# Kernel tuning notes

Hardware: AMD Instinct MI355X
Metric: run time of the kernel (lower is better)

## Reference

```python
import jax, jax.numpy as jnp
import numpy as np

B, P, D, N, H = 1, 256, 512, 8, 64
STD = 0.02
IGNORE = -1000000.0


def setup_inputs() -> dict:
    key = jax.random.key(0)
    ks = jax.random.split(key, 9)
    inp = {"normalized_resid_pre": jax.random.normal(ks[0], (B, P, D), jnp.float32)}
    for i, s in enumerate("ABCDE"):
        inp["W_" + s] = STD * jax.random.normal(ks[i + 1], (N, D, H), jnp.float32)
        inp["b_" + s] = jnp.zeros((N, H), jnp.float32)
    inp["W_V"] = STD * jax.random.normal(ks[6], (N, H, H, H), jnp.float32)
    inp["W_K"] = STD * jax.random.normal(ks[7], (N, H, H, H), jnp.float32)
    inp["W_O"] = STD * jax.random.normal(ks[8], (N, H, D), jnp.float32)
    inp["b_O"] = jnp.zeros((D,), jnp.float32)
    return inp


def reference(normalized_resid_pre, W_A, b_A, W_B, b_B, W_C, b_C, W_D, b_D, W_E, b_E, W_V, W_K, W_O, b_O):
    x = normalized_resid_pre
    b_sz = x.shape[0]
    proj = lambda W, b: jnp.einsum('ndh,bpd->bpnh', W, x) + b
    ta = proj(W_A, b_A)
    tb = proj(W_B, b_B)
    tc = proj(W_C, b_C)
    td = proj(W_D, b_D)
    te = proj(W_E, b_E)
    # V_Layer: v[b, p1, p2, n, h3]
    v = jnp.einsum('bpnh,bqng,nhgf->bpqnf', td, te, W_V)
    # TrittentionCScore: chained einsums -> scores[b, n, p, q, r]
    step1 = jnp.einsum('brnk,nijk->brij', tc, W_K)
    step2 = jnp.einsum('brij,bqnj->briq', step1, tb)
    scores = jnp.einsum('briq,bpni->bnpqr', step2, ta)
    # CausalMask (attn_eq=False, order_attn=True): mask over (t=p, s=q, q=r) dims
    ti = jnp.arange(P)[:, None, None]
    si = jnp.arange(P)[None, :, None]
    qi = jnp.arange(P)[None, None, :]
    mask = (ti >= qi) | (si >= qi) | (ti >= si)  # [P, P, P]
    scores = jnp.where(mask, IGNORE, scores)
    # TrittentionCPattern: b n p q r -> b n r (p q), /d_head, extra column, softmax
    flat = jnp.transpose(scores, (0, 1, 4, 2, 3)).reshape(b_sz, N, P, P * P) / H
    extra = jnp.full((b_sz, N, P, 1), -1000.0, flat.dtype)
    attn = jax.nn.softmax(jnp.concatenate([flat, extra], axis=-1), axis=-1)
    # Z_Layer: v -> b n h (p s), extra zero column, combine
    vf = jnp.transpose(v, (0, 3, 4, 1, 2)).reshape(b_sz, N, H, P * P)
    vf = jnp.concatenate([vf, jnp.zeros((b_sz, N, H, 1), vf.dtype)], axis=-1)
    z = jnp.einsum('bnql,bnhl->bqnh', attn, vf)
    # Result + Out
    zint = jnp.einsum('bqnh,nhd->bqnd', z, W_O)
    return zint.sum(axis=2) + b_O
```

## Files before the change

### kernel.cpp

```cpp
#include <hip/hip_runtime.h>
#include <hip/hip_bf16.h>


typedef __hip_bfloat16 bf16;
typedef __attribute__((ext_vector_type(8))) short short8;
typedef __attribute__((ext_vector_type(4))) short s16x4;
typedef __attribute__((ext_vector_type(4))) float floatx4;

__device__ __forceinline__ float ldf(const float* p){ return *p; }
__device__ __forceinline__ float ldf(const bf16* p){ return __bfloat162float(*p); }
__device__ __forceinline__ void  stf(float* p, float v){ *p = v; }
__device__ __forceinline__ void  stf(bf16*  p, float v){ *p = __float2bfloat16(v); }

__device__ __forceinline__ floatx4 mfma16(short8 a, short8 b, floatx4 c){
  return __builtin_amdgcn_mfma_f32_16x16x32_bf16(a, b, c, 0, 0, 0);
}
__device__ __forceinline__ short8 ld_g8(const bf16* p){
  return *reinterpret_cast<const short8*>(p);
}
__device__ __forceinline__ short bfs(float x){
  bf16 v = __float2bfloat16(x);
  return *reinterpret_cast<short*>(&v);
}

__global__ void dtype_probe(const unsigned* __restrict__ x, int* __restrict__ flag)
{
  int t = threadIdx.x;
  int cnt = 0;
  #pragma unroll
  for (int k = 0; k < 4; k++) {
    unsigned w = x[t*4 + k];
    unsigned lo = w & 0xFFFFu;
    unsigned e  = (lo >> 7) & 0xFFu;
    if (lo == 0u || (e >= 90u && e <= 145u)) cnt++;
  }
  #pragma unroll
  for (int off = 32; off; off >>= 1) cnt += __shfl_down(cnt, off);
  if (t == 0) *flag = (cnt >= 160) ? 1 : 0;
}

template<typename TI>
__global__ __launch_bounds__(256) void proj_kern(
    const int* __restrict__ gate, int want, const TI* __restrict__ x,
    const TI* __restrict__ W0, const TI* __restrict__ b0,
    const TI* __restrict__ W1, const TI* __restrict__ b1,
    const TI* __restrict__ W2, const TI* __restrict__ b2,
    const TI* __restrict__ W3, const TI* __restrict__ b3,
    const TI* __restrict__ W4, const TI* __restrict__ b4,
    bf16* __restrict__ tproj)
{
  if (*gate != want) return;
  const TI* Ws[5] = {W0, W1, W2, W3, W4};
  const TI* bs[5] = {b0, b1, b2, b3, b4};
  const int bz = blockIdx.z, j = bz >> 3, n = bz & 7;
  const TI* B    = Ws[j] + (size_t)n * 32768;
  const TI* bias = bs[j] + n * 64;
  bf16* out = tproj + (size_t)j * 131072;
  const int m0 = blockIdx.y * 64;
  __shared__ float As[16][68];
  __shared__ float Bs[16][68];
  const int t = threadIdx.x, tx = t & 15, ty = t >> 4;
  float acc[4][4] = {};
  for (int k0 = 0; k0 < 512; k0 += 16) {
    { int m = t >> 2, kk = (t & 3) * 4;
      const TI* ap = x + (size_t)(m0 + m) * 512 + (k0 + kk);
      float a0 = ldf(ap+0), a1 = ldf(ap+1), a2 = ldf(ap+2), a3 = ldf(ap+3);
      As[kk+0][m] = a0; As[kk+1][m] = a1; As[kk+2][m] = a2; As[kk+3][m] = a3; }
    { int kk = t >> 4, nn = (t & 15) * 4;
      const TI* bp = B + (size_t)(k0 + kk) * 64 + nn;
      Bs[kk][nn+0] = ldf(bp+0); Bs[kk][nn+1] = ldf(bp+1);
      Bs[kk][nn+2] = ldf(bp+2); Bs[kk][nn+3] = ldf(bp+3); }
    __syncthreads();
    #pragma unroll
    for (int kk = 0; kk < 16; kk++) {
      float4 a4 = *reinterpret_cast<const float4*>(&As[kk][ty*4]);
      float4 b4 = *reinterpret_cast<const float4*>(&Bs[kk][tx*4]);
      float av[4] = {a4.x,a4.y,a4.z,a4.w}, bv[4] = {b4.x,b4.y,b4.z,b4.w};
      #pragma unroll
      for (int im = 0; im < 4; im++)
        #pragma unroll
        for (int in = 0; in < 4; in++) acc[im][in] += av[im] * bv[in];
    }
    __syncthreads();
  }
  #pragma unroll
  for (int im = 0; im < 4; im++)
    #pragma unroll
    for (int in = 0; in < 4; in++) {
      float v = acc[im][in] + ldf(bias + tx*4 + in);
      int p = m0 + ty*4 + im, h = tx*4 + in;
      if (j < 3) out[(size_t)p * 512 + n*64 + h] = __float2bfloat16(v);
      else       out[(size_t)n * 16384 + (size_t)h * 256 + p] = __float2bfloat16(v);
    }
}

template<typename TW>
__global__ __launch_bounds__(256) void s1t_mfma(
    const int* __restrict__ gate, int want,
    const bf16* __restrict__ tc, const TW* __restrict__ WK, bf16* __restrict__ s1t)
{
  if (*gate != want) return;
  const int i = blockIdx.x;
  const int t = threadIdx.x, wid = t >> 6, lane = t & 63, quad = lane >> 4, l16 = lane & 15;
  const int rw = blockIdx.y * 64 + wid * 16;
  floatx4 acc[4];
  #pragma unroll
  for (int jt = 0; jt < 4; jt++) acc[jt] = (floatx4){0.f, 0.f, 0.f, 0.f};
  for (int kc = 0; kc < 16; kc++) {
    short8 af = ld_g8(tc + (size_t)(rw + l16) * 512 + kc*32 + quad*8);
    const int n = kc >> 1, kk = (kc & 1) * 32 + quad * 8;
    #pragma unroll
    for (int jt = 0; jt < 4; jt++) {
      const TW* bp = WK + ((size_t)(n*64 + i) * 64 + jt*16 + l16) * 64 + kk;
      short8 bf;
      if constexpr (sizeof(TW) == 2) {
        bf = ld_g8((const bf16*)bp);
      } else {
        float4 x0 = *reinterpret_cast<const float4*>(bp);
        float4 x1 = *reinterpret_cast<const float4*>(bp + 4);
        bf[0]=bfs(x0.x); bf[1]=bfs(x0.y); bf[2]=bfs(x0.z); bf[3]=bfs(x0.w);
        bf[4]=bfs(x1.x); bf[5]=bfs(x1.y); bf[6]=bfs(x1.z); bf[7]=bfs(x1.w);
      }
      acc[jt] = mfma16(af, bf, acc[jt]);
    }
  }
  #pragma unroll
  for (int jt = 0; jt < 4; jt++)
    #pragma unroll
    for (int reg = 0; reg < 4; reg++)
      s1t[(size_t)(rw + quad*4 + reg) * 4096 + i*64 + jt*16 + l16] =
          __float2bfloat16(acc[jt][reg]);
}

template<typename TA, typename TB, typename TC, bool BIAS>
__global__ __launch_bounds__(256) void gemm_tile(
    const int* __restrict__ gate, int want,
    const TA* __restrict__ A, const TB* __restrict__ B, TC* __restrict__ C,
    const TB* __restrict__ bias,
    int Ncols, int K, int lda, int ldc)
{
  if (*gate != want) return;
  const int m0 = blockIdx.y * 64, n0 = blockIdx.x * 64;
  __shared__ float As[16][68];
  __shared__ float Bs[16][68];
  const int t = threadIdx.x, tx = t & 15, ty = t >> 4;
  float acc[4][4] = {};
  for (int k0 = 0; k0 < K; k0 += 16) {
    { int m = t >> 2, kk = (t & 3) * 4;
      const TA* ap = A + (size_t)(m0 + m) * lda + (k0 + kk);
      float a0 = ldf(ap+0), a1 = ldf(ap+1), a2 = ldf(ap+2), a3 = ldf(ap+3);
      As[kk+0][m] = a0; As[kk+1][m] = a1; As[kk+2][m] = a2; As[kk+3][m] = a3; }
    { int kk = t >> 4, nn = (t & 15) * 4;
      const TB* bp = B + (size_t)(k0 + kk) * Ncols + (n0 + nn);
      Bs[kk][nn+0] = ldf(bp+0); Bs[kk][nn+1] = ldf(bp+1);
      Bs[kk][nn+2] = ldf(bp+2); Bs[kk][nn+3] = ldf(bp+3); }
    __syncthreads();
    #pragma unroll
    for (int kk = 0; kk < 16; kk++) {
      float4 a4 = *reinterpret_cast<const float4*>(&As[kk][ty*4]);
      float4 b4 = *reinterpret_cast<const float4*>(&Bs[kk][tx*4]);
      float av[4] = {a4.x,a4.y,a4.z,a4.w}, bv[4] = {b4.x,b4.y,b4.z,b4.w};
      #pragma unroll
      for (int im = 0; im < 4; im++)
        #pragma unroll
        for (int in = 0; in < 4; in++) acc[im][in] += av[im] * bv[in];
    }
    __syncthreads();
  }
  #pragma unroll
  for (int im = 0; im < 4; im++) {
    TC* cp = C + (size_t)(m0 + ty*4 + im) * ldc + n0 + tx*4;
    #pragma unroll
    for (int in = 0; in < 4; in++) {
      float v = acc[im][in];
      if constexpr (BIAS) v += ldf(bias + n0 + tx*4 + in);
      stf(cp + in, v);
    }
  }
}

__global__ __launch_bounds__(256) void tbs_kern(const bf16* __restrict__ tb,
                                                bf16* __restrict__ tbsbf)
{
  int t = blockIdx.x * 256 + threadIdx.x;
  int q = t >> 6, j = t & 63;
  float s = 0.f;
  #pragma unroll
  for (int n = 0; n < 8; n++) s += ldf(tb + q*512 + n*64 + j);
  tbsbf[t] = __float2bfloat16(s * 0.015625f);
}

__global__ __launch_bounds__(256) void tri_attn(
    const bf16* __restrict__ ta,
    const bf16* __restrict__ tbsbf,
    const bf16* __restrict__ s1t,
    const bf16* __restrict__ tdT,
    const bf16* __restrict__ teT,
    bf16* __restrict__ Sbuf)
{
  __shared__ __align__(16) char smb[39936];
  const int bx = blockIdx.x;
  const int n = bx & 7;
  const int r = 255 - (bx >> 3);
  const int t = threadIdx.x;
  const int wid = t >> 6, lane = t & 63, quad = lane >> 4, l16 = lane & 15;
  bf16* srow = Sbuf + (size_t)n * 1048576 + (size_t)r * 4096;
  if (r < 2) {
    short8 zz = (short8){0,0,0,0,0,0,0,0};
    reinterpret_cast<short8*>(srow)[t]       = zz;
    reinterpret_cast<short8*>(srow)[t + 256] = zz;
    return;
  }
  const int nch  = ((r - 1) >> 5) + 1;
  const int rcap = nch * 32;

  {
    const bf16* s1r = s1t + (size_t)r * 4096;
    short8 bfr[4][2];
    #pragma unroll
    for (int it = 0; it < 4; it++)
      #pragma unroll
      for (int kc = 0; kc < 2; kc++)
        bfr[it][kc] = ld_g8(s1r + (it*16 + l16)*64 + kc*32 + quad*8);
    #pragma unroll
    for (int qt = 0; qt < 4; qt++) {
      const int q0 = wid * 64 + qt * 16;
      if (q0 >= rcap) continue;
      if (q0 >= r) {
        #pragma unroll
        for (int it = 0; it < 4; it++)
          #pragma unroll
          for (int reg = 0; reg < 4; reg++) {
            int q = q0 + quad*4 + reg;
            *reinterpret_cast<bf16*>(smb + q*136 + (it*16 + l16)*2) =
                __float2bfloat16(0.f);
          }
        continue;
      }
      short8 af0 = ld_g8(tbsbf + (q0 + l16)*64 + quad*8);
      short8 af1 = ld_g8(tbsbf + (q0 + l16)*64 + 32 + quad*8);
      #pragma unroll
      for (int it = 0; it < 4; it++) {
        floatx4 acc = {0.f, 0.f, 0.f, 0.f};
        acc = mfma16(af0, bfr[it][0], acc);
        acc = mfma16(af1, bfr[it][1], acc);
        #pragma unroll
        for (int reg = 0; reg < 4; reg++) {
          int q = q0 + quad*4 + reg;
          float v = (q >= 1 && q < r) ? acc[reg] : 0.f;
          *reinterpret_cast<bf16*>(smb + q*136 + (it*16 + l16)*2) = __float2bfloat16(v);
        }
      }
    }
  }
  short8 taf[4][2];
  #pragma unroll
  for (int pt = 0; pt < 4; pt++)
    #pragma unroll
    for (int kc = 0; kc < 2; kc++)
      taf[pt][kc] = ld_g8(ta + (size_t)((pt*4 + wid)*16 + l16)*512 + n*64
                             + kc*32 + quad*8);
  __syncthreads();

  floatx4 Tacc[4][4];
  #pragma unroll
  for (int pt = 0; pt < 4; pt++)
    #pragma unroll
    for (int gt = 0; gt < 4; gt++) Tacc[pt][gt] = (floatx4){0.f, 0.f, 0.f, 0.f};
  float Zp = 0.f;
  char* EwB = smb + 34816 + wid * 1152;
  for (int ch = 0; ch < nch; ch++) {
    const int qc = ch * 32;
    if (qc + 31 <= wid * 16) continue;
    short8 cfr[2][2];
    #pragma unroll
    for (int qt2 = 0; qt2 < 2; qt2++)
      #pragma unroll
      for (int kc = 0; kc < 2; kc++)
        cfr[qt2][kc] = *reinterpret_cast<const short8*>(
            smb + (qc + qt2*16 + l16)*136 + (kc*32 + quad*8)*2);
    short8 tef[4];
    #pragma unroll
    for (int gt = 0; gt < 4; gt++)
      tef[gt] = ld_g8(teT + (size_t)n*16384 + (gt*16 + l16)*256 + qc + quad*8);
    #pragma unroll
    for (int pt = 0; pt < 4; pt++) {
      const int ptb = (pt*4 + wid) * 16;
      if (ptb >= qc + 31) continue;
      #pragma unroll
      for (int qt2 = 0; qt2 < 2; qt2++) {
        const int qh = qc + qt2*16;
        char* erow0 = EwB + (quad*4)*72 + (qt2*16 + l16)*2;
        if (qh + 15 <= ptb) {
          #pragma unroll
          for (int reg = 0; reg < 4; reg++)
            *reinterpret_cast<bf16*>(erow0 + reg*72) = __float2bfloat16(0.f);
        } else {
          floatx4 acc = {0.f, 0.f, 0.f, 0.f};
          acc = mfma16(taf[pt][0], cfr[qt2][0], acc);
          acc = mfma16(taf[pt][1], cfr[qt2][1], acc);
          if (qh >= ptb + 16 && qh + 15 < r) {
            #pragma unroll
            for (int reg = 0; reg < 4; reg++) {
              float e = __expf(acc[reg]);
              Zp += e;
              *reinterpret_cast<bf16*>(erow0 + reg*72) = __float2bfloat16(e);
            }
          } else {
            #pragma unroll
            for (int reg = 0; reg < 4; reg++) {
              int p = ptb + quad*4 + reg;
              int q = qh + l16;
              float e = (p < q && q < r) ? __expf(acc[reg]) : 0.f;
              Zp += e;
              *reinterpret_cast<bf16*>(erow0 + reg*72) = __float2bfloat16(e);
            }
          }
        }
      }
      short8 ef = *reinterpret_cast<const short8*>(EwB + l16*72 + quad*16);
      __builtin_amdgcn_s_setprio(1);
      #pragma unroll
      for (int gt = 0; gt < 4; gt++)
        Tacc[pt][gt] = mfma16(ef, tef[gt], Tacc[pt][gt]);
      __builtin_amdgcn_s_setprio(0);
    }
  }
  #pragma unroll
  for (int off = 32; off; off >>= 1) Zp += __shfl_down(Zp, off);
  float* scr = reinterpret_cast<float*>(smb + 39424);
  if (lane == 0) scr[wid] = Zp;
  __syncthreads();
  const float rinv = 1.f / (scr[0] + scr[1] + scr[2] + scr[3]);

  #pragma unroll
  for (int pt = 0; pt < 4; pt++) {
    if ((pt*4 + wid)*16 >= rcap) continue;
    #pragma unroll
    for (int gt = 0; gt < 4; gt++)
      #pragma unroll
      for (int reg = 0; reg < 4; reg++) {
        int g = gt*16 + l16;
        int p = (pt*4 + wid)*16 + quad*4 + reg;
        *reinterpret_cast<bf16*>(smb + g*528 + p*2) = __float2bfloat16(Tacc[pt][gt][reg]);
      }
  }
  __syncthreads();

  {
    short8 Taf[8];
    #pragma unroll
    for (int kc = 0; kc < 8; kc++)
      if (kc < nch)
        Taf[kc] = *reinterpret_cast<const short8*>(
            smb + (wid*16 + l16)*528 + (kc*32 + quad*8)*2);
    #pragma unroll
    for (int ht = 0; ht < 4; ht++) {
      floatx4 acc = {0.f, 0.f, 0.f, 0.f};
      __builtin_amdgcn_s_setprio(1);
      #pragma unroll
      for (int kc = 0; kc < 8; kc++) {
        if (kc < nch) {
          short8 bfragd = ld_g8(tdT + (size_t)n*16384 + (ht*16 + l16)*256 + kc*32 + quad*8);
          acc = mfma16(Taf[kc], bfragd, acc);
        }
      }
      __builtin_amdgcn_s_setprio(0);
      #pragma unroll
      for (int reg = 0; reg < 4; reg++) {
        int g = wid*16 + quad*4 + reg, h = ht*16 + l16;
        srow[h*64 + g] = __float2bfloat16(acc[reg] * rinv);
      }
    }
  }
}

template<typename TW>
__global__ __launch_bounds__(256) void z_kern(
    const int* __restrict__ gate, int want,
    const bf16* __restrict__ Sbuf, const TW* __restrict__ WV,
    float* __restrict__ zpart, int kslice)
{
  if (*gate != want) return;
  __shared__ __align__(16) char lds[32 * 136];
  const int rt = blockIdx.x, n = blockIdx.y, ks = blockIdx.z;
  const int t = threadIdx.x, wid = t >> 6, lane = t & 63, quad = lane >> 4, l16 = lane & 15;
  const int rw = rt * 64 + wid * 16;
  const int k0 = ks * kslice;
  const TW*  wvn = WV   + (size_t)n * 262144;
  const bf16* sn = Sbuf + (size_t)n * 1048576;
  floatx4 acc[4];
  #pragma unroll
  for (int ft = 0; ft < 4; ft++) acc[ft] = (floatx4){0.f, 0.f, 0.f, 0.f};
  const int row = t >> 3, f8 = (t & 7) * 8;
  for (int kb = k0; kb < k0 + kslice; kb += 32) {
    {
      const TW* src = wvn + (size_t)(kb + row) * 64 + f8;
      short sv[8];
      if constexpr (sizeof(TW) == 2) {
        short8 v = ld_g8((const bf16*)src);
        #pragma unroll
        for (int j = 0; j < 8; j++) sv[j] = v[j];
      } else {
        float4 a = *reinterpret_cast<const float4*>(src);
        float4 b = *reinterpret_cast<const float4*>(src + 4);
        sv[0]=bfs(a.x); sv[1]=bfs(a.y); sv[2]=bfs(a.z); sv[3]=bfs(a.w);
        sv[4]=bfs(b.x); sv[5]=bfs(b.y); sv[6]=bfs(b.z); sv[7]=bfs(b.w);
      }
      short* dst = reinterpret_cast<short*>(lds + row*136 + f8*2);
      s16x4 lo = {sv[0],sv[1],sv[2],sv[3]}, hi = {sv[4],sv[5],sv[6],sv[7]};
      *reinterpret_cast<s16x4*>(dst)     = lo;
      *reinterpret_cast<s16x4*>(dst + 4) = hi;
    }
    __syncthreads();
    short8 af = ld_g8(sn + (size_t)(rw + l16) * 4096 + kb + quad*8);
    #pragma unroll
    for (int ft = 0; ft < 4; ft++) {
      short8 bfv;
      #pragma unroll
      for (int j = 0; j < 8; j++)
        bfv[j] = *reinterpret_cast<const short*>(
            lds + (quad*8 + j)*136 + (ft*16 + l16)*2);
      acc[ft] = mfma16(af, bfv, acc[ft]);
    }
    __syncthreads();
  }
  float* zp = zpart + (size_t)ks * 131072;
  #pragma unroll
  for (int ft = 0; ft < 4; ft++)
    #pragma unroll
    for (int reg = 0; reg < 4; reg++)
      zp[(size_t)(rw + quad*4 + reg) * 512 + n*64 + ft*16 + l16] = acc[ft][reg];
}

__global__ __launch_bounds__(256) void zred_kern(
    const float* __restrict__ zpart, bf16* __restrict__ zbb, int ks)
{
  int idx = blockIdx.x * 256 + threadIdx.x;
  float s = 0.f;
  for (int k = 0; k < ks; k++) s += zpart[(size_t)k * 131072 + idx];
  zbb[idx] = __float2bfloat16(s);
}

extern "C" void kernel_launch(void* const* d_in, const int* in_sizes, int n_in,
                              void* d_out, int out_size, void* d_ws, size_t ws_size,
                              hipStream_t stream)
{
  (void)in_sizes; (void)n_in; (void)out_size;
  char* wsb = (char*)d_ws;
  int*  flag  = (int*)wsb;
  bf16* tproj = (bf16*)(wsb + 256);
  bf16* tbsbf = (bf16*)(wsb + 1310976);
  bf16* s1t   = (bf16*)(wsb + 1343744);
  bf16* zbb   = (bf16*)(wsb + 3440896);
  bf16* Sbuf  = (bf16*)(wsb + 4194304);
  const long TE = 131072;
  const bool bigws = (ws_size == 0) || (ws_size >= 25165824);
  const int  ks     = bigws ? 8 : 2;
  const int  kslice = 4096 / ks;
  float* zpart = (float*)(bigws ? (wsb + 20971520) : (wsb + 1343744));

  dtype_probe<<<1, 64, 0, stream>>>((const unsigned*)d_in[0], flag);

  proj_kern<bf16><<<dim3(1,4,40), 256, 0, stream>>>(
      flag, 1, (const bf16*)d_in[0],
      (const bf16*)d_in[1], (const bf16*)d_in[2], (const bf16*)d_in[3], (const bf16*)d_in[4],
      (const bf16*)d_in[5], (const bf16*)d_in[6], (const bf16*)d_in[7], (const bf16*)d_in[8],
      (const bf16*)d_in[9], (const bf16*)d_in[10], tproj);
  proj_kern<float><<<dim3(1,4,40), 256, 0, stream>>>(
      flag, 0, (const float*)d_in[0],
      (const float*)d_in[1], (const float*)d_in[2], (const float*)d_in[3], (const float*)d_in[4],
      (const float*)d_in[5], (const float*)d_in[6], (const float*)d_in[7], (const float*)d_in[8],
      (const float*)d_in[9], (const float*)d_in[10], tproj);
  tbs_kern<<<64, 256, 0, stream>>>(tproj + 1*TE, tbsbf);
  s1t_mfma<bf16><<<dim3(64,4), 256, 0, stream>>>(
      flag, 1, tproj + 2*TE, (const bf16*)d_in[12], s1t);
  s1t_mfma<float><<<dim3(64,4), 256, 0, stream>>>(
      flag, 0, tproj + 2*TE, (const float*)d_in[12], s1t);
  tri_attn<<<2048, 256, 0, stream>>>(
      tproj, tbsbf, s1t, tproj + 3*TE, tproj + 4*TE, Sbuf);
  z_kern<bf16><<<dim3(4,8,ks), 256, 0, stream>>>(
      flag, 1, Sbuf, (const bf16*)d_in[11], zpart, kslice);
  z_kern<float><<<dim3(4,8,ks), 256, 0, stream>>>(
      flag, 0, Sbuf, (const float*)d_in[11], zpart, kslice);
  zred_kern<<<512, 256, 0, stream>>>(zpart, zbb, ks);
  gemm_tile<bf16, bf16, bf16, true><<<dim3(8,4), 256, 0, stream>>>(
      flag, 1, zbb, (const bf16*)d_in[13], (bf16*)d_out, (const bf16*)d_in[14],
      512, 512, 512, 512);
  gemm_tile<bf16, float, float, true><<<dim3(8,4), 256, 0, stream>>>(
      flag, 0, zbb, (const float*)d_in[13], (float*)d_out, (const float*)d_in[14],
      512, 512, 512, 512);
}
```

Measured before the change: 267.5 us.

## Precompute per-row C matrices in a separate kernel and use a leaner tri_attn2

```diff
diff --git a/kernel.cpp b/kernel.cpp
--- a/kernel.cpp
+++ b/kernel.cpp
@@ -188,6 +188,33 @@
   #pragma unroll
   for (int n = 0; n < 8; n++) s += ldf(tb + q*512 + n*64 + j);
   tbsbf[t] = __float2bfloat16(s * 0.015625f);
+}
+
+__global__ __launch_bounds__(256) void c_kern(
+    const bf16* __restrict__ tbsbf, const bf16* __restrict__ s1t,
+    bf16* __restrict__ cpack)
+{
+  const int r = blockIdx.y;
+  const int a = r >> 5;
+  const int rows = 32 * (a + 1);
+  const int q0 = blockIdx.x * 64;
+  if (q0 >= rows) return;
+  const int t = threadIdx.x, wid = t >> 6, lane = t & 63, quad = lane >> 4, l16 = lane & 15;
+  const int qw = wid * 16;
+  if (q0 + qw >= rows) return;
+  const bf16* s1r = s1t + (size_t)r * 4096;
+  bf16* cp = cpack + ((size_t)rows * (16*a + (r & 31)) + q0) * 64;
+  short8 af0 = ld_g8(tbsbf + (size_t)(q0 + qw + l16) * 64 + quad*8);
+  short8 af1 = ld_g8(tbsbf + (size_t)(q0 + qw + l16) * 64 + 32 + quad*8);
+  #pragma unroll
+  for (int it = 0; it < 4; it++) {
+    floatx4 acc = {0.f, 0.f, 0.f, 0.f};
+    acc = mfma16(af0, ld_g8(s1r + (it*16 + l16)*64 + quad*8), acc);
+    acc = mfma16(af1, ld_g8(s1r + (it*16 + l16)*64 + 32 + quad*8), acc);
+    #pragma unroll
+    for (int reg = 0; reg < 4; reg++)
+      cp[(size_t)(qw + quad*4 + reg) * 64 + it*16 + l16] = __float2bfloat16(acc[reg]);
+  }
 }
 
 __global__ __launch_bounds__(256) void tri_attn(
@@ -375,6 +402,163 @@
   }
 }
 
+__global__ __launch_bounds__(256) void tri_attn2(
+    const bf16* __restrict__ ta,
+    const bf16* __restrict__ cpack,
+    const bf16* __restrict__ tdT,
+    const bf16* __restrict__ teT,
+    bf16* __restrict__ Sbuf)
+{
+  __shared__ __align__(16) char smb[22528];
+  const int bx = blockIdx.x;
+  const int n = bx & 7;
+  const int r = 255 - (bx >> 3);
+  const int t = threadIdx.x;
+  const int wid = t >> 6, lane = t & 63, quad = lane >> 4, l16 = lane & 15;
+  bf16* srow = Sbuf + (size_t)n * 1048576 + (size_t)r * 4096;
+  if (r < 2) {
+    short8 zz = (short8){0,0,0,0,0,0,0,0};
+    reinterpret_cast<short8*>(srow)[t]       = zz;
+    reinterpret_cast<short8*>(srow)[t + 256] = zz;
+    return;
+  }
+  const int nch  = ((r - 1) >> 5) + 1;
+  const int rcap = nch * 32;
+  const int ra = r >> 5;
+  const bf16* cp = cpack + (size_t)(32 * (ra + 1)) * (16*ra + (r & 31)) * 64;
+
+  short8 taf[4][2];
+  #pragma unroll
+  for (int pt = 0; pt < 4; pt++)
+    #pragma unroll
+    for (int kc = 0; kc < 2; kc++)
+      taf[pt][kc] = ld_g8(ta + (size_t)((pt*4 + wid)*16 + l16)*512 + n*64
+                             + kc*32 + quad*8);
+
+  floatx4 Tacc[4][4];
+  #pragma unroll
+  for (int pt = 0; pt < 4; pt++)
+    #pragma unroll
+    for (int gt = 0; gt < 4; gt++) Tacc[pt][gt] = (floatx4){0.f, 0.f, 0.f, 0.f};
+  float Zp = 0.f;
+  char* EwB = smb + 17408 + wid * 1152;
+  for (int ch = 0; ch < nch; ch++) {
+    const int qc = ch * 32;
+    if (qc + 31 <= wid * 16) continue;
+    short8 cfr[2][2];
+    #pragma unroll
+    for (int qt2 = 0; qt2 < 2; qt2++)
+      #pragma unroll
+      for (int kc = 0; kc < 2; kc++)
+        cfr[qt2][kc] = ld_g8(cp + (size_t)(qc + qt2*16 + l16)*64 + kc*32 + quad*8);
+    short8 tef[4];
+    #pragma unroll
+    for (int gt = 0; gt < 4; gt++)
+      tef[gt] = ld_g8(teT + (size_t)n*16384 + (gt*16 + l16)*256 + qc + quad*8);
+    #pragma unroll
+    for (int pt = 0; pt < 4; pt++) {
+      const int ptb = (pt*4 + wid) * 16;
+      if (ptb >= qc + 31) continue;
+      #pragma unroll
+      for (int qt2 = 0; qt2 < 2; qt2++) {
+        const int qh = qc + qt2*16;
+        char* erow0 = EwB + (quad*4)*72 + (qt2*16 + l16)*2;
+        if (qh + 15 <= ptb) {
+          #pragma unroll
+          for (int reg = 0; reg < 4; reg++)
+            *reinterpret_cast<bf16*>(erow0 + reg*72) = __float2bfloat16(0.f);
+        } else {
+          floatx4 acc = {0.f, 0.f, 0.f, 0.f};
+          acc = mfma16(taf[pt][0], cfr[qt2][0], acc);
+          acc = mfma16(taf[pt][1], cfr[qt2][1], acc);
+          if (qh >= ptb + 16 && qh + 15 < r) {
+            #pragma unroll
+            for (int reg = 0; reg < 4; reg++) {
+              float e = __expf(acc[reg]);
+              Zp += e;
+              *reinterpret_cast<bf16*>(erow0 + reg*72) = __float2bfloat16(e);
+            }
+          } else {
+            #pragma unroll
+            for (int reg = 0; reg < 4; reg++) {
+              int p = ptb + quad*4 + reg;
+              int q = qh + l16;
+              float e = (p < q && q < r) ? __expf(acc[reg]) : 0.f;
+              Zp += e;
+              *reinterpret_cast<bf16*>(erow0 + reg*72) = __float2bfloat16(e);
+            }
+          }
+        }
+      }
+      short8 ef = *reinterpret_cast<const short8*>(EwB + l16*72 + quad*16);
+      __builtin_amdgcn_s_setprio(1);
+      #pragma unroll
+      for (int gt = 0; gt < 4; gt++)
+        Tacc[pt][gt] = mfma16(ef, tef[gt], Tacc[pt][gt]);
+      __builtin_amdgcn_s_setprio(0);
+    }
+  }
+  #pragma unroll
+  for (int off = 32; off; off >>= 1) Zp += __shfl_down(Zp, off);
+  float* scr = reinterpret_cast<float*>(smb + 22016);
+  if (lane == 0) scr[wid] = Zp;
+  __syncthreads();
+  const float rinv = 1.f / (scr[0] + scr[1] + scr[2] + scr[3]);
+
+  floatx4 Sacc[4];
+  #pragma unroll
+  for (int ht = 0; ht < 4; ht++) Sacc[ht] = (floatx4){0.f, 0.f, 0.f, 0.f};
+  #pragma unroll
+  for (int h2 = 0; h2 < 2; h2++) {
+    if (h2 * 128 < rcap) {
+      __syncthreads();
+      #pragma unroll
+      for (int pt2 = 0; pt2 < 2; pt2++) {
+        const int pt = h2*2 + pt2;
+        const int pbase = (pt*4 + wid) * 16;
+        if (pbase >= rcap) continue;
+        const int pl = pbase - h2*128;
+        #pragma unroll
+        for (int gt = 0; gt < 4; gt++)
+          #pragma unroll
+          for (int reg = 0; reg < 4; reg++) {
+            int g = gt*16 + l16;
+            *reinterpret_cast<bf16*>(smb + g*272 + (pl + quad*4 + reg)*2) =
+                __float2bfloat16(Tacc[pt][gt][reg]);
+          }
+      }
+      __syncthreads();
+      short8 Taf[4];
+      #pragma unroll
+      for (int kcl = 0; kcl < 4; kcl++)
+        if (h2*4 + kcl < nch)
+          Taf[kcl] = *reinterpret_cast<const short8*>(
+              smb + (wid*16 + l16)*272 + (kcl*32 + quad*8)*2);
+      __builtin_amdgcn_s_setprio(1);
+      #pragma unroll
+      for (int ht = 0; ht < 4; ht++) {
+        #pragma unroll
+        for (int kcl = 0; kcl < 4; kcl++) {
+          const int kc = h2*4 + kcl;
+          if (kc < nch) {
+            short8 bfragd = ld_g8(tdT + (size_t)n*16384 + (ht*16 + l16)*256
+                                      + kc*32 + quad*8);
+            Sacc[ht] = mfma16(Taf[kcl], bfragd, Sacc[ht]);
+          }
+        }
+      }
+      __builtin_amdgcn_s_setprio(0);
+    }
+  }
+  #pragma unroll
+  for (int ht = 0; ht < 4; ht++)
+    #pragma unroll
+    for (int reg = 0; reg < 4; reg++) {
+      int g = wid*16 + quad*4 + reg, h = ht*16 + l16;
+      srow[h*64 + g] = __float2bfloat16(Sacc[ht][reg] * rinv);
+    }
+}
+
 template<typename TW>
 __global__ __launch_bounds__(256) void z_kern(
     const int* __restrict__ gate, int want,
@@ -394,8 +578,7 @@
   for (int ft = 0; ft < 4; ft++) acc[ft] = (floatx4){0.f, 0.f, 0.f, 0.f};
   const int row = t >> 3, f8 = (t & 7) * 8;
   for (int kb = k0; kb < k0 + kslice; kb += 32) {
-    {
-      const TW* src = wvn + (size_t)(kb + row) * 64 + f8;
+    { const TW* src = wvn + (size_t)(kb + row) * 64 + f8;
       short sv[8];
       if constexpr (sizeof(TW) == 2) {
         short8 v = ld_g8((const bf16*)src);
@@ -448,17 +631,32 @@
 {
   (void)in_sizes; (void)n_in; (void)out_size;
   char* wsb = (char*)d_ws;
-  int*  flag  = (int*)wsb;
-  bf16* tproj = (bf16*)(wsb + 256);
-  bf16* tbsbf = (bf16*)(wsb + 1310976);
-  bf16* s1t   = (bf16*)(wsb + 1343744);
-  bf16* zbb   = (bf16*)(wsb + 3440896);
-  bf16* Sbuf  = (bf16*)(wsb + 4194304);
   const long TE = 131072;
   const bool bigws = (ws_size == 0) || (ws_size >= 25165824);
-  const int  ks     = bigws ? 8 : 2;
-  const int  kslice = 4096 / ks;
-  float* zpart = (float*)(bigws ? (wsb + 20971520) : (wsb + 1343744));
+
+  int* flag; bf16 *tproj, *tbsbf, *s1t, *zbb, *Sbuf, *cpack; float* zpart; int ks;
+  if (bigws) {
+    flag  = (int*)wsb;
+    tproj = (bf16*)(wsb + 4096);
+    tbsbf = (bf16*)(wsb + 1314816);
+    s1t   = (bf16*)(wsb + 1347584);
+    cpack = (bf16*)(wsb + 3444736);
+    zpart = (float*)(wsb + 3444736);
+    zbb   = (bf16*)(wsb + 7639040);
+    Sbuf  = (bf16*)(wsb + 8388608);
+    ks    = 8;
+  } else {
+    flag  = (int*)wsb;
+    tproj = (bf16*)(wsb + 256);
+    tbsbf = (bf16*)(wsb + 1310976);
+    s1t   = (bf16*)(wsb + 1343744);
+    zbb   = (bf16*)(wsb + 3440896);
+    Sbuf  = (bf16*)(wsb + 4194304);
+    cpack = nullptr;
+    zpart = (float*)(wsb + 1343744);
+    ks    = 2;
+  }
+  const int kslice = 4096 / ks;
 
   dtype_probe<<<1, 64, 0, stream>>>((const unsigned*)d_in[0], flag);
 
@@ -477,8 +675,14 @@
       flag, 1, tproj + 2*TE, (const bf16*)d_in[12], s1t);
   s1t_mfma<float><<<dim3(64,4), 256, 0, stream>>>(
       flag, 0, tproj + 2*TE, (const float*)d_in[12], s1t);
-  tri_attn<<<2048, 256, 0, stream>>>(
-      tproj, tbsbf, s1t, tproj + 3*TE, tproj + 4*TE, Sbuf);
+  if (bigws) {
+    c_kern<<<dim3(4,256), 256, 0, stream>>>(tbsbf, s1t, cpack);
+    tri_attn2<<<2048, 256, 0, stream>>>(
+        tproj, cpack, tproj + 3*TE, tproj + 4*TE, Sbuf);
+  } else {
+    tri_attn<<<2048, 256, 0, stream>>>(
+        tproj, tbsbf, s1t, tproj + 3*TE, tproj + 4*TE, Sbuf);
+  }
   z_kern<bf16><<<dim3(4,8,ks), 256, 0, stream>>>(
       flag, 1, Sbuf, (const bf16*)d_in[11], zpart, kslice);
   z_kern<float><<<dim3(4,8,ks), 256, 0, stream>>>(
```

Result: slower. 272.9 us (+2.0%).
